# Performance work log

Hardware: AMD Instinct MI355X
Metric: run time of the kernel (lower is better)

Reference implementation:

```python
import jax, jax.numpy as jnp
from jax import lax
import numpy as np

B, L, D = 16, 512, 256
F, K = 256, 3
M = 2048
EPS = 1e-5


def setup_inputs() -> dict:
    key = jax.random.key(0)
    ks = jax.random.split(key, 12)
    x = jax.random.normal(ks[0], (B, L, D), jnp.float32)
    # integer durations >= 1, sum over L <= 3*512 = 1536 < M, as in training targets
    target = jax.random.randint(ks[1], (B, L), 1, 4)
    s = 0.02
    conv1_w = jax.random.normal(ks[2], (F, D, K), jnp.float32) * s
    conv1_b = jnp.zeros((F,), jnp.float32)
    ln1_g = jnp.ones((F,), jnp.float32)
    ln1_b = jnp.zeros((F,), jnp.float32)
    conv2_w = jax.random.normal(ks[3], (F, F, K), jnp.float32) * s
    conv2_b = jnp.zeros((F,), jnp.float32)
    ln2_g = jnp.ones((F,), jnp.float32)
    ln2_b = jnp.zeros((F,), jnp.float32)
    lin_w = jax.random.normal(ks[4], (F, 1), jnp.float32) * s
    lin_b = jnp.zeros((1,), jnp.float32)
    return dict(x=x, target=target, mel_max_length=M,
                conv1_w=conv1_w, conv1_b=conv1_b, ln1_g=ln1_g, ln1_b=ln1_b,
                conv2_w=conv2_w, conv2_b=conv2_b, ln2_g=ln2_g, ln2_b=ln2_b,
                lin_w=lin_w, lin_b=lin_b)


def _layer_norm(h, g, b):
    mu = jnp.mean(h, axis=-1, keepdims=True)
    var = jnp.mean(jnp.square(h - mu), axis=-1, keepdims=True)
    return (h - mu) * lax.rsqrt(var + EPS) * g + b


def _conv1d(h_bld, w, b):
    # h: (B, L, C_in), w: (C_out, C_in, K) -> (B, L, C_out), SAME padding
    pad = (w.shape[-1] - 1) // 2
    h = jnp.transpose(h_bld, (0, 2, 1))  # (B, C, L)
    h = lax.conv_general_dilated(h, w, (1,), [(pad, pad)],
                                 dimension_numbers=('NCH', 'OIH', 'NCH'))
    return jnp.transpose(h + b[None, :, None], (0, 2, 1))


def _duration_predictor(x, conv1_w, conv1_b, ln1_g, ln1_b,
                        conv2_w, conv2_b, ln2_g, ln2_b, lin_w, lin_b):
    # FastSpeech duration predictor (eval mode: dropout = identity)
    h = jax.nn.relu(_layer_norm(_conv1d(x, conv1_w, conv1_b), ln1_g, ln1_b))
    h = jax.nn.relu(_layer_norm(_conv1d(h, conv2_w, conv2_b), ln2_g, ln2_b))
    return jax.nn.relu(h @ lin_w + lin_b)[..., 0]  # (B, L)


def _length_regulate(x, dur, mel_max_length):
    # alignment[b,m,l] = 1 iff cs[l-1] <= m < cs[l]  (exactly the scatter+diff trick
    # of create_alignment, padded to mel_max_length as in the original F.pad)
    cs = jnp.cumsum(dur, axis=1)              # (B, L) inclusive cumsum
    prev = cs - dur                           # exclusive cumsum
    m = jnp.arange(mel_max_length)[None, :, None]  # (1, M, 1)
    align = ((m >= prev[:, None, :]) & (m < cs[:, None, :])).astype(x.dtype)  # (B,M,L)
    return jnp.einsum('bml,bld->bmd', align, x)


def reference(x, target, mel_max_length, conv1_w, conv1_b, ln1_g, ln1_b,
              conv2_w, conv2_b, ln2_g, ln2_b, lin_w, lin_b):
    dup = _duration_predictor(x, conv1_w, conv1_b, ln1_g, ln1_b,
                              conv2_w, conv2_b, ln2_g, ln2_b, lin_w, lin_b)
    output = _length_regulate(x, target, mel_max_length)
    return (output, dup)
```

## Files before the change

### kernel.cpp

```cpp
#include <hip/hip_runtime.h>
#include <hip/hip_bf16.h>

#define Bn 16
#define Ln 512
#define Cn 256
#define Fn 256
#define Kn 3
#define Mn 2048

#define NKSTEP 24
#define MT 32
#define XS_PS 264
#define NCONVBLK 256
#define NGATH_HALF 4096

typedef __attribute__((ext_vector_type(8))) short short8;
typedef __attribute__((ext_vector_type(4))) float f32x4;

static __device__ __forceinline__ unsigned short f2bf(float f) {
    unsigned int u = __float_as_uint(f);
    return (unsigned short)((u + 0x7fff + ((u >> 16) & 1)) >> 16);
}

__global__ __launch_bounds__(256) void pack_scan(
    const float* __restrict__ w1, const float* __restrict__ w2,
    unsigned short* __restrict__ bp1, unsigned short* __restrict__ bp2,
    const int* __restrict__ target, int* __restrict__ map)
{
    __shared__ int ss[256];
    const int blk = blockIdx.x;
    const int t = threadIdx.x;
    if (blk < 1536) {
        int i = blk * 256 + t;
        const float* w = w1;
        unsigned short* bp = bp1;
        if (i >= Fn * Cn * Kn) { i -= Fn * Cn * Kn; w = w2; bp = bp2; }
        int j    = i & 7;
        int lane = (i >> 3) & 63;
        int nt   = (i >> 9) & 15;
        int s    = i >> 13;
        int kap = s * 32 + ((lane >> 4) * 8) + j;
        int k = kap >> 8;
        int d = kap & 255;
        int f = nt * 16 + (lane & 15);
        bp[i] = f2bf(w[(f * Cn + d) * Kn + k]);
    } else {
        int b = blk - 1536;
        int v0 = target[b * Ln + 2 * t];
        int v1 = target[b * Ln + 2 * t + 1];
        ss[t] = v0 + v1;
        __syncthreads();
        for (int off = 1; off < 256; off <<= 1) {
            int add = (t >= off) ? ss[t - off] : 0;
            __syncthreads();
            ss[t] += add;
            __syncthreads();
        }
        int S     = ss[t];
        int total = ss[255];
        int cs1   = S;
        int cs0   = S - v1;
        int prev0 = cs0 - v0;
        for (int m = prev0; m < cs0; ++m) map[b * Mn + m] = 2 * t;
        for (int m = cs0;   m < cs1; ++m) map[b * Mn + m] = 2 * t + 1;
        for (int m = total + t; m < Mn; m += 256) map[b * Mn + m] = -1;
    }
}

template <bool IS_F32_IN, bool DO_LINEAR, bool WITH_AUX>
__global__ __launch_bounds__(256) void conv_mfma(
    const void* __restrict__ in_,
    const unsigned short* __restrict__ bp,
    const float* __restrict__ bias,
    const float* __restrict__ gamma,
    const float* __restrict__ beta,
    const float* __restrict__ lw,
    const float* __restrict__ lb,
    unsigned short* __restrict__ hout,
    float* __restrict__ dup,
    const float* __restrict__ gx,
    const int* __restrict__ gmap,
    float* __restrict__ gout,
    int gofs)
{
    __shared__ __align__(16) unsigned short xs[(MT + 2) * XS_PS];
    __shared__ float2 red[MT][4];
    __shared__ float  red2[MT][4];

    const int t = threadIdx.x;

    if (WITH_AUX && blockIdx.x >= NCONVBLK) {
        int e4 = (blockIdx.x - NCONVBLK) * 256 + t + gofs;
        int d4 = e4 & 63;
        int bm = e4 >> 6;
        int b  = bm >> 11;
        int l  = gmap[bm];
        float4 val = make_float4(0.f, 0.f, 0.f, 0.f);
        if (l >= 0) val = *((const float4*)(gx + (size_t)(b * Ln + l) * Cn) + d4);
        ((float4*)gout)[e4] = val;
        return;
    }

    const int b  = blockIdx.x >> 4;
    const int l0 = (blockIdx.x & 15) * MT;

    if (IS_F32_IN) {
        const float* in = (const float*)in_;
        for (int idx = t; idx < (MT + 2) * 64; idx += 256) {
            int row = idx >> 6;
            int c4  = (idx & 63) * 4;
            int l = l0 + row - 1;
            float4 v = make_float4(0.f, 0.f, 0.f, 0.f);
            if (l >= 0 && l < Ln) v = *(const float4*)&in[((size_t)b * Ln + l) * Cn + c4];
            unsigned int lo = (unsigned int)f2bf(v.x) | ((unsigned int)f2bf(v.y) << 16);
            unsigned int hi = (unsigned int)f2bf(v.z) | ((unsigned int)f2bf(v.w) << 16);
            *(uint2*)&xs[row * XS_PS + c4] = make_uint2(lo, hi);
        }
    } else {
        const unsigned short* in = (const unsigned short*)in_;
        for (int idx = t; idx < (MT + 2) * 32; idx += 256) {
            int row = idx >> 5;
            int c8  = (idx & 31) * 8;
            int l = l0 + row - 1;
            uint4 v = make_uint4(0u, 0u, 0u, 0u);
            if (l >= 0 && l < Ln) v = *(const uint4*)&in[((size_t)b * Ln + l) * Cn + c8];
            *(uint4*)&xs[row * XS_PS + c8] = v;
        }
    }
    __syncthreads();

    const int lane = t & 63;
    const int wv   = t >> 6;
    const int mrow = lane & 15;
    const int q    = lane >> 4;

    f32x4  acc[2][4] = {};
    short8 bfr[2][4];
    short8 afr[2][2];

    auto loadB = [&](int s, int slot) {
        const unsigned short* p = bp + (size_t)((s * 16 + wv * 4) * 64 + lane) * 8;
        #pragma unroll
        for (int i = 0; i < 4; ++i)
            bfr[slot][i] = *(const short8*)(p + (size_t)i * 64 * 8);
    };
    auto loadA = [&](int s, int slot) {
        const int k    = s >> 3;
        const int dcol = (s & 7) * 32 + q * 8;
        #pragma unroll
        for (int mt = 0; mt < 2; ++mt)
            afr[slot][mt] = *(const short8*)&xs[(mt * 16 + mrow + k) * XS_PS + dcol];
    };

    loadB(0, 0); loadA(0, 0);
    loadB(1, 1); loadA(1, 1);

    #pragma unroll 2
    for (int s = 0; s < NKSTEP; ++s) {
        const int slot = s & 1;
        #pragma unroll
        for (int mt = 0; mt < 2; ++mt)
            #pragma unroll
            for (int i = 0; i < 4; ++i)
                acc[mt][i] = __builtin_amdgcn_mfma_f32_16x16x32_bf16(
                    afr[slot][mt], bfr[slot][i], acc[mt][i], 0, 0, 0);
        const int sn = (s + 2 < NKSTEP) ? (s + 2) : s;
        loadB(sn, slot);
        loadA(sn, slot);
    }

    float gv[4], bv[4], lwv[4], biasv[4];
    #pragma unroll
    for (int i = 0; i < 4; ++i) {
        int col = wv * 64 + i * 16 + mrow;
        biasv[i] = bias[col];
        gv[i]    = gamma[col];
        bv[i]    = beta[col];
        if (DO_LINEAR) lwv[i] = lw[col];
    }
    #pragma unroll
    for (int mt = 0; mt < 2; ++mt)
        #pragma unroll
        for (int i = 0; i < 4; ++i)
            #pragma unroll
            for (int r = 0; r < 4; ++r)
                acc[mt][i][r] += biasv[i];

    #pragma unroll
    for (int mt = 0; mt < 2; ++mt)
        #pragma unroll
        for (int r = 0; r < 4; ++r) {
            float s  = acc[mt][0][r] + acc[mt][1][r] + acc[mt][2][r] + acc[mt][3][r];
            float sq = acc[mt][0][r] * acc[mt][0][r] + acc[mt][1][r] * acc[mt][1][r]
                     + acc[mt][2][r] * acc[mt][2][r] + acc[mt][3][r] * acc[mt][3][r];
            #pragma unroll
            for (int off = 1; off <= 8; off <<= 1) {
                s  += __shfl_xor(s,  off, 64);
                sq += __shfl_xor(sq, off, 64);
            }
            if (mrow == 0) red[mt * 16 + q * 4 + r][wv] = make_float2(s, sq);
        }
    __syncthreads();

    float muv[2][4], rsv[2][4];
    #pragma unroll
    for (int mt = 0; mt < 2; ++mt)
        #pragma unroll
        for (int r = 0; r < 4; ++r) {
            int row = mt * 16 + q * 4 + r;
            float2 p0 = red[row][0], p1 = red[row][1], p2 = red[row][2], p3 = red[row][3];
            float s  = p0.x + p1.x + p2.x + p3.x;
            float sq = p0.y + p1.y + p2.y + p3.y;
            float mu  = s * (1.f / 256.f);
            float var = sq * (1.f / 256.f) - mu * mu;
            muv[mt][r] = mu;
            rsv[mt][r] = rsqrtf(var + 1e-5f);
        }

    if (!DO_LINEAR) {
        #pragma unroll
        for (int mt = 0; mt < 2; ++mt)
            #pragma unroll
            for (int r = 0; r < 4; ++r) {
                int l = l0 + mt * 16 + q * 4 + r;
                size_t base = ((size_t)b * Ln + l) * Fn;
                #pragma unroll
                for (int i = 0; i < 4; ++i) {
                    float o = fmaxf((acc[mt][i][r] - muv[mt][r]) * rsv[mt][r] * gv[i] + bv[i], 0.f);
                    hout[base + wv * 64 + i * 16 + mrow] = f2bf(o);
                }
            }
    } else {
        #pragma unroll
        for (int mt = 0; mt < 2; ++mt)
            #pragma unroll
            for (int r = 0; r < 4; ++r) {
                float dot = 0.f;
                #pragma unroll
                for (int i = 0; i < 4; ++i) {
                    float o = fmaxf((acc[mt][i][r] - muv[mt][r]) * rsv[mt][r] * gv[i] + bv[i], 0.f);
                    dot += o * lwv[i];
                }
                #pragma unroll
                for (int off = 1; off <= 8; off <<= 1)
                    dot += __shfl_xor(dot, off, 64);
                if (mrow == 0) red2[mt * 16 + q * 4 + r][wv] = dot;
            }
        __syncthreads();
        if (t < MT) {
            float d = red2[t][0] + red2[t][1] + red2[t][2] + red2[t][3];
            dup[b * Ln + l0 + t] = fmaxf(d + lb[0], 0.f);
        }
    }
}

extern "C" void kernel_launch(void* const* d_in, const int* in_sizes, int n_in,
                              void* d_out, int out_size, void* d_ws, size_t ws_size,
                              hipStream_t stream) {
    const float* x    = (const float*)d_in[0];
    const int*   targ = (const int*)d_in[1];
    const float* c1w = (const float*)d_in[3];
    const float* c1b = (const float*)d_in[4];
    const float* g1  = (const float*)d_in[5];
    const float* be1 = (const float*)d_in[6];
    const float* c2w = (const float*)d_in[7];
    const float* c2b = (const float*)d_in[8];
    const float* g2  = (const float*)d_in[9];
    const float* be2 = (const float*)d_in[10];
    const float* lw  = (const float*)d_in[11];
    const float* lb  = (const float*)d_in[12];

    float* out     = (float*)d_out;
    float* out_dup = out + (size_t)Bn * Mn * Cn;

    char* ws = (char*)d_ws;
    unsigned short* bp1 = (unsigned short*)ws;
    unsigned short* bp2 = (unsigned short*)(ws + 393216);
    unsigned short* h1  = (unsigned short*)(ws + 2 * 393216);
    int*            map = (int*)(ws + 2 * 393216 + 4194304);

    pack_scan<<<1552, 256, 0, stream>>>(c1w, c2w, bp1, bp2, targ, map);

    conv_mfma<true, false, true><<<NCONVBLK + NGATH_HALF, 256, 0, stream>>>(
        (const void*)x, bp1, c1b, g1, be1, nullptr, nullptr, h1, nullptr,
        x, map, out, 0);

    conv_mfma<false, true, true><<<NCONVBLK + NGATH_HALF, 256, 0, stream>>>(
        (const void*)h1, bp2, c2b, g2, be2, lw, lb, nullptr, out_dup,
        x, map, out, NGATH_HALF * 256);
}
```

Measured before the change: 118.0 us.

## Use 512-thread blocks with 8 waves splitting conv output columns

Doubles the block size from 256 to 512 threads in all kernels. In the conv kernel each of 8 waves now computes 32 output channels instead of 64, so per-wave accumulator and B-fragment registers are halved, and LayerNorm reductions now combine 8 partials. The scan now uses one thread per token, and the gather blocks are halved in count with each covering twice as many elements. This is meant to raise occupancy and MFMA latency hiding, at the cost of more A-fragment LDS reads per useful MFMA and a larger cross-wave reduction.

```diff
diff --git a/kernel.cpp b/kernel.cpp
--- a/kernel.cpp
+++ b/kernel.cpp
@@ -12,7 +12,7 @@
 #define MT 32
 #define XS_PS 264
 #define NCONVBLK 256
-#define NGATH_HALF 4096
+#define NGATH_HALF 2048
 
 typedef __attribute__((ext_vector_type(8))) short short8;
 typedef __attribute__((ext_vector_type(4))) float f32x4;
@@ -22,53 +22,55 @@
     return (unsigned short)((u + 0x7fff + ((u >> 16) & 1)) >> 16);
 }
 
-__global__ __launch_bounds__(256) void pack_scan(
+static __device__ __forceinline__ void pack_one(const float* __restrict__ w,
+                                                unsigned short* __restrict__ bp,
+                                                int i) {
+    int j    = i & 7;
+    int lane = (i >> 3) & 63;
+    int nt   = (i >> 9) & 15;
+    int s    = i >> 13;
+    int kap = s * 32 + ((lane >> 4) * 8) + j;
+    int k = kap >> 8;
+    int d = kap & 255;
+    int f = nt * 16 + (lane & 15);
+    bp[i] = f2bf(w[(f * Cn + d) * Kn + k]);
+}
+
+__global__ __launch_bounds__(512) void pack_scan(
     const float* __restrict__ w1, const float* __restrict__ w2,
     unsigned short* __restrict__ bp1, unsigned short* __restrict__ bp2,
     const int* __restrict__ target, int* __restrict__ map)
 {
-    __shared__ int ss[256];
+    __shared__ int ss[Ln];
     const int blk = blockIdx.x;
     const int t = threadIdx.x;
-    if (blk < 1536) {
-        int i = blk * 256 + t;
+    if (blk < 768) {
+        int i = blk * 512 + t;
         const float* w = w1;
         unsigned short* bp = bp1;
         if (i >= Fn * Cn * Kn) { i -= Fn * Cn * Kn; w = w2; bp = bp2; }
-        int j    = i & 7;
-        int lane = (i >> 3) & 63;
-        int nt   = (i >> 9) & 15;
-        int s    = i >> 13;
-        int kap = s * 32 + ((lane >> 4) * 8) + j;
-        int k = kap >> 8;
-        int d = kap & 255;
-        int f = nt * 16 + (lane & 15);
-        bp[i] = f2bf(w[(f * Cn + d) * Kn + k]);
-    } else {
-        int b = blk - 1536;
-        int v0 = target[b * Ln + 2 * t];
-        int v1 = target[b * Ln + 2 * t + 1];
-        ss[t] = v0 + v1;
+        pack_one(w, bp, i);
+        return;
+    }
+    int b = blk - 768;
+    int v = target[b * Ln + t];
+    ss[t] = v;
+    __syncthreads();
+    for (int off = 1; off < Ln; off <<= 1) {
+        int add = (t >= off) ? ss[t - off] : 0;
         __syncthreads();
-        for (int off = 1; off < 256; off <<= 1) {
-            int add = (t >= off) ? ss[t - off] : 0;
-            __syncthreads();
-            ss[t] += add;
-            __syncthreads();
-        }
-        int S     = ss[t];
-        int total = ss[255];
-        int cs1   = S;
-        int cs0   = S - v1;
-        int prev0 = cs0 - v0;
-        for (int m = prev0; m < cs0; ++m) map[b * Mn + m] = 2 * t;
-        for (int m = cs0;   m < cs1; ++m) map[b * Mn + m] = 2 * t + 1;
-        for (int m = total + t; m < Mn; m += 256) map[b * Mn + m] = -1;
-    }
+        ss[t] += add;
+        __syncthreads();
+    }
+    int cs    = ss[t];
+    int prev  = cs - v;
+    int total = ss[Ln - 1];
+    for (int m = prev; m < cs; ++m) map[b * Mn + m] = t;
+    for (int m = total + t; m < Mn; m += Ln) map[b * Mn + m] = -1;
 }
 
 template <bool IS_F32_IN, bool DO_LINEAR, bool WITH_AUX>
-__global__ __launch_bounds__(256) void conv_mfma(
+__global__ __launch_bounds__(512) void conv_mfma(
     const void* __restrict__ in_,
     const unsigned short* __restrict__ bp,
     const float* __restrict__ bias,
@@ -84,13 +86,13 @@
     int gofs)
 {
     __shared__ __align__(16) unsigned short xs[(MT + 2) * XS_PS];
-    __shared__ float2 red[MT][4];
-    __shared__ float  red2[MT][4];
+    __shared__ float2 red[MT][8];
+    __shared__ float  red2[MT][8];
 
     const int t = threadIdx.x;
 
     if (WITH_AUX && blockIdx.x >= NCONVBLK) {
-        int e4 = (blockIdx.x - NCONVBLK) * 256 + t + gofs;
+        int e4 = (blockIdx.x - NCONVBLK) * 512 + t + gofs;
         int d4 = e4 & 63;
         int bm = e4 >> 6;
         int b  = bm >> 11;
@@ -106,7 +108,7 @@
 
     if (IS_F32_IN) {
         const float* in = (const float*)in_;
-        for (int idx = t; idx < (MT + 2) * 64; idx += 256) {
+        for (int idx = t; idx < (MT + 2) * 64; idx += 512) {
             int row = idx >> 6;
             int c4  = (idx & 63) * 4;
             int l = l0 + row - 1;
@@ -118,7 +120,7 @@
         }
     } else {
         const unsigned short* in = (const unsigned short*)in_;
-        for (int idx = t; idx < (MT + 2) * 32; idx += 256) {
+        for (int idx = t; idx < (MT + 2) * 32; idx += 512) {
             int row = idx >> 5;
             int c8  = (idx & 31) * 8;
             int l = l0 + row - 1;
@@ -134,65 +136,61 @@
     const int mrow = lane & 15;
     const int q    = lane >> 4;
 
-    f32x4  acc[2][4] = {};
-    short8 bfr[2][4];
-    short8 afr[2][2];
-
-    auto loadB = [&](int s, int slot) {
-        const unsigned short* p = bp + (size_t)((s * 16 + wv * 4) * 64 + lane) * 8;
-        #pragma unroll
-        for (int i = 0; i < 4; ++i)
-            bfr[slot][i] = *(const short8*)(p + (size_t)i * 64 * 8);
-    };
-    auto loadA = [&](int s, int slot) {
-        const int k    = s >> 3;
-        const int dcol = (s & 7) * 32 + q * 8;
-        #pragma unroll
-        for (int mt = 0; mt < 2; ++mt)
-            afr[slot][mt] = *(const short8*)&xs[(mt * 16 + mrow + k) * XS_PS + dcol];
-    };
-
-    loadB(0, 0); loadA(0, 0);
-    loadB(1, 1); loadA(1, 1);
-
-    #pragma unroll 2
-    for (int s = 0; s < NKSTEP; ++s) {
-        const int slot = s & 1;
-        #pragma unroll
-        for (int mt = 0; mt < 2; ++mt)
-            #pragma unroll
-            for (int i = 0; i < 4; ++i)
-                acc[mt][i] = __builtin_amdgcn_mfma_f32_16x16x32_bf16(
-                    afr[slot][mt], bfr[slot][i], acc[mt][i], 0, 0, 0);
-        const int sn = (s + 2 < NKSTEP) ? (s + 2) : s;
-        loadB(sn, slot);
-        loadA(sn, slot);
-    }
-
-    float gv[4], bv[4], lwv[4], biasv[4];
-    #pragma unroll
-    for (int i = 0; i < 4; ++i) {
-        int col = wv * 64 + i * 16 + mrow;
-        biasv[i] = bias[col];
-        gv[i]    = gamma[col];
-        bv[i]    = beta[col];
-        if (DO_LINEAR) lwv[i] = lw[col];
-    }
+    f32x4 acc00 = {}, acc01 = {}, acc10 = {}, acc11 = {};
+    short8 a0_0, a1_0, b0_0, b1_0;
+    short8 a0_1, a1_1, b0_1, b1_1;
+
+#define LOADB(B0, B1, s_) { \
+    const unsigned short* p_ = bp + (size_t)((((s_) * 16) + wv * 2) * 64 + lane) * 8; \
+    B0 = *(const short8*)p_; \
+    B1 = *(const short8*)(p_ + 512); }
+#define LOADA(A0, A1, s_) { \
+    const int k_ = (s_) >> 3; \
+    const int dc_ = ((s_) & 7) * 32 + q * 8; \
+    A0 = *(const short8*)&xs[(mrow + k_) * XS_PS + dc_]; \
+    A1 = *(const short8*)&xs[(16 + mrow + k_) * XS_PS + dc_]; }
+#define DOMFMA(A0, A1, B0, B1) { \
+    acc00 = __builtin_amdgcn_mfma_f32_16x16x32_bf16(A0, B0, acc00, 0, 0, 0); \
+    acc01 = __builtin_amdgcn_mfma_f32_16x16x32_bf16(A0, B1, acc01, 0, 0, 0); \
+    acc10 = __builtin_amdgcn_mfma_f32_16x16x32_bf16(A1, B0, acc10, 0, 0, 0); \
+    acc11 = __builtin_amdgcn_mfma_f32_16x16x32_bf16(A1, B1, acc11, 0, 0, 0); }
+
+    LOADB(b0_0, b1_0, 0) LOADA(a0_0, a1_0, 0)
+    LOADB(b0_1, b1_1, 1) LOADA(a0_1, a1_1, 1)
+
+    #pragma unroll
+    for (int s = 0; s < NKSTEP; s += 2) {
+        DOMFMA(a0_0, a1_0, b0_0, b1_0)
+        if (s + 2 < NKSTEP) { LOADB(b0_0, b1_0, s + 2) LOADA(a0_0, a1_0, s + 2) }
+        DOMFMA(a0_1, a1_1, b0_1, b1_1)
+        if (s + 3 < NKSTEP) { LOADB(b0_1, b1_1, s + 3) LOADA(a0_1, a1_1, s + 3) }
+    }
+#undef LOADB
+#undef LOADA
+#undef DOMFMA
+
+    const int c0 = wv * 32 + mrow;
+    const int c1 = c0 + 16;
+    float bias0 = bias[c0], bias1 = bias[c1];
+    float g0 = gamma[c0], g1g = gamma[c1];
+    float be0 = beta[c0], be1 = beta[c1];
+    float lw0 = 0.f, lw1 = 0.f;
+    if (DO_LINEAR) { lw0 = lw[c0]; lw1 = lw[c1]; }
+
+    #pragma unroll
+    for (int r = 0; r < 4; ++r) {
+        acc00[r] += bias0; acc01[r] += bias1;
+        acc10[r] += bias0; acc11[r] += bias1;
+    }
+
     #pragma unroll
     for (int mt = 0; mt < 2; ++mt)
         #pragma unroll
-        for (int i = 0; i < 4; ++i)
-            #pragma unroll
-            for (int r = 0; r < 4; ++r)
-                acc[mt][i][r] += biasv[i];
-
-    #pragma unroll
-    for (int mt = 0; mt < 2; ++mt)
-        #pragma unroll
         for (int r = 0; r < 4; ++r) {
-            float s  = acc[mt][0][r] + acc[mt][1][r] + acc[mt][2][r] + acc[mt][3][r];
-            float sq = acc[mt][0][r] * acc[mt][0][r] + acc[mt][1][r] * acc[mt][1][r]
-                     + acc[mt][2][r] * acc[mt][2][r] + acc[mt][3][r] * acc[mt][3][r];
+            float v0 = mt ? acc10[r] : acc00[r];
+            float v1 = mt ? acc11[r] : acc01[r];
+            float s  = v0 + v1;
+            float sq = v0 * v0 + v1 * v1;
             #pragma unroll
             for (int off = 1; off <= 8; off <<= 1) {
                 s  += __shfl_xor(s,  off, 64);
@@ -208,9 +206,12 @@
         #pragma unroll
         for (int r = 0; r < 4; ++r) {
             int row = mt * 16 + q * 4 + r;
-            float2 p0 = red[row][0], p1 = red[row][1], p2 = red[row][2], p3 = red[row][3];
-            float s  = p0.x + p1.x + p2.x + p3.x;
-            float sq = p0.y + p1.y + p2.y + p3.y;
+            float s = 0.f, sq = 0.f;
+            #pragma unroll
+            for (int w = 0; w < 8; ++w) {
+                float2 p = red[row][w];
+                s += p.x; sq += p.y;
+            }
             float mu  = s * (1.f / 256.f);
             float var = sq * (1.f / 256.f) - mu * mu;
             muv[mt][r] = mu;
@@ -222,25 +223,25 @@
         for (int mt = 0; mt < 2; ++mt)
             #pragma unroll
             for (int r = 0; r < 4; ++r) {
+                float v0 = mt ? acc10[r] : acc00[r];
+                float v1 = mt ? acc11[r] : acc01[r];
                 int l = l0 + mt * 16 + q * 4 + r;
                 size_t base = ((size_t)b * Ln + l) * Fn;
-                #pragma unroll
-                for (int i = 0; i < 4; ++i) {
-                    float o = fmaxf((acc[mt][i][r] - muv[mt][r]) * rsv[mt][r] * gv[i] + bv[i], 0.f);
-                    hout[base + wv * 64 + i * 16 + mrow] = f2bf(o);
-                }
+                float o0 = fmaxf((v0 - muv[mt][r]) * rsv[mt][r] * g0  + be0, 0.f);
+                float o1 = fmaxf((v1 - muv[mt][r]) * rsv[mt][r] * g1g + be1, 0.f);
+                hout[base + c0] = f2bf(o0);
+                hout[base + c1] = f2bf(o1);
             }
     } else {
         #pragma unroll
         for (int mt = 0; mt < 2; ++mt)
             #pragma unroll
             for (int r = 0; r < 4; ++r) {
-                float dot = 0.f;
-                #pragma unroll
-                for (int i = 0; i < 4; ++i) {
-                    float o = fmaxf((acc[mt][i][r] - muv[mt][r]) * rsv[mt][r] * gv[i] + bv[i], 0.f);
-                    dot += o * lwv[i];
-                }
+                float v0 = mt ? acc10[r] : acc00[r];
+                float v1 = mt ? acc11[r] : acc01[r];
+                float o0 = fmaxf((v0 - muv[mt][r]) * rsv[mt][r] * g0  + be0, 0.f);
+                float o1 = fmaxf((v1 - muv[mt][r]) * rsv[mt][r] * g1g + be1, 0.f);
+                float dot = o0 * lw0 + o1 * lw1;
                 #pragma unroll
                 for (int off = 1; off <= 8; off <<= 1)
                     dot += __shfl_xor(dot, off, 64);
@@ -248,7 +249,9 @@
             }
         __syncthreads();
         if (t < MT) {
-            float d = red2[t][0] + red2[t][1] + red2[t][2] + red2[t][3];
+            float d = 0.f;
+            #pragma unroll
+            for (int w = 0; w < 8; ++w) d += red2[t][w];
             dup[b * Ln + l0 + t] = fmaxf(d + lb[0], 0.f);
         }
     }
@@ -279,13 +282,13 @@
     unsigned short* h1  = (unsigned short*)(ws + 2 * 393216);
     int*            map = (int*)(ws + 2 * 393216 + 4194304);
 
-    pack_scan<<<1552, 256, 0, stream>>>(c1w, c2w, bp1, bp2, targ, map);
-
-    conv_mfma<true, false, true><<<NCONVBLK + NGATH_HALF, 256, 0, stream>>>(
+    pack_scan<<<784, 512, 0, stream>>>(c1w, c2w, bp1, bp2, targ, map);
+
+    conv_mfma<true, false, true><<<NCONVBLK + NGATH_HALF, 512, 0, stream>>>(
         (const void*)x, bp1, c1b, g1, be1, nullptr, nullptr, h1, nullptr,
         x, map, out, 0);
 
-    conv_mfma<false, true, true><<<NCONVBLK + NGATH_HALF, 256, 0, stream>>>(
+    conv_mfma<false, true, true><<<NCONVBLK + NGATH_HALF, 512, 0, stream>>>(
         (const void*)h1, bp2, c2b, g2, be2, lw, lb, nullptr, out_dup,
-        x, map, out, NGATH_HALF * 256);
-}
+        x, map, out, NGATH_HALF * 512);
+}
```

Result: slower. 122.0 us (+3.4%).
